# Optimization experiments

Measured on AMD Instinct MI355X. Metric: run time of the kernel, lower is better.

The kernel has to match this reference:

```python
import jax, jax.numpy as jnp
import numpy as np

K = 3  # inferred kernel size (28->26->pool->13->11->pool->5 matches 32*5*5 FC input)


def _patches(x, k=K):
    # x: (N,C,H,W) -> (N,C,k*k,OH,OW) valid patches, stride 1
    N, C, H, W = x.shape
    OH, OW = H - k + 1, W - k + 1
    return jnp.stack(
        [x[:, :, i:i + OH, j:j + OW] for i in range(k) for j in range(k)], axis=2
    )


def _maxpool2(x):
    N, C, H, W = x.shape
    H2, W2 = H // 2, W // 2
    x = x[:, :, :H2 * 2, :W2 * 2].reshape(N, C, H2, 2, W2, 2)
    return x.max(axis=(3, 5))


def _lc2d(x, w, b):
    # unshared-weight locally connected conv: w (O,C,k*k,OH,OW), b (O,OH,OW)
    p = _patches(x)  # (N,C,k*k,OH,OW)
    return jnp.einsum('nckij,ockij->noij', p, w) + b


def setup_inputs():
    key = jax.random.key(0)
    ks = jax.random.split(key, 9)
    s = 0.05
    return {
        'x': jax.random.normal(ks[0], (4096, 1, 28, 28), jnp.float32),
        'w1': jax.random.normal(ks[1], (16, 1, 9, 26, 26), jnp.float32) * s,
        'b1': jax.random.normal(ks[2], (16, 26, 26), jnp.float32) * s,
        'w2': jax.random.normal(ks[3], (32, 16, 9, 11, 11), jnp.float32) * s,
        'b2': jax.random.normal(ks[4], (32, 11, 11), jnp.float32) * s,
        'fc1_w': jax.random.normal(ks[5], (32 * 5 * 5, 128), jnp.float32) * s,
        'fc1_b': jax.random.normal(ks[6], (128,), jnp.float32) * s,
        'fc2_w': jax.random.normal(ks[7], (128, 10), jnp.float32) * s,
        'fc2_b': jax.random.normal(ks[8], (10,), jnp.float32) * s,
    }


def reference(x, w1, b1, w2, b2, fc1_w, fc1_b, fc2_w, fc2_b):
    h = _maxpool2(jax.nn.relu(_lc2d(x, w1, b1)))      # (N,16,13,13)
    h = _maxpool2(jax.nn.relu(_lc2d(h, w2, b2)))      # (N,32,5,5)
    h = h.reshape(h.shape[0], -1)                      # (N,800)
    h = jax.nn.relu(h @ fc1_w + fc1_b)                 # (N,128)
    return h @ fc2_w + fc2_b                           # (N,10)
```

## Files before the change

### kernel.cpp

```cpp
#include <hip/hip_runtime.h>

#define NB 4096

typedef __attribute__((ext_vector_type(8))) short s8v;
typedef __attribute__((ext_vector_type(4))) float f4v;

#define XB_OFF  0u
#define H1B_OFF 6422528u
#define H2B_OFF 28573696u
#define W2B_OFF 35127296u
#define B2R_OFF 36765696u
#define W1B_OFF 36778496u
#define B1R_OFF 37470720u
#define WFB_OFF 37513984u

__device__ __forceinline__ unsigned short f2bf(float f) {
  unsigned int u = __builtin_bit_cast(unsigned int, f);
  u += 0x7fffu + ((u >> 16) & 1u);
  return (unsigned short)(u >> 16);
}

__global__ __launch_bounds__(256) void k_prep(const float* __restrict__ x,
                                              const float* __restrict__ w1,
                                              const float* __restrict__ b1,
                                              const float* __restrict__ w2,
                                              const float* __restrict__ b2,
                                              const float* __restrict__ f1w,
                                              short* __restrict__ xB,
                                              short* __restrict__ w1b,
                                              float* __restrict__ b1r,
                                              short* __restrict__ w2b,
                                              float* __restrict__ b2r,
                                              short* __restrict__ wfb) {
  const int bx = blockIdx.x;
  if (bx < 3200) {
    __shared__ float t[32][33];
    const int c0 = (bx % 25) * 32;
    const int n0 = (bx / 25) * 32;
    const int tx = threadIdx.x & 31, ty = threadIdx.x >> 5;
    #pragma unroll
    for (int i = 0; i < 32; i += 8) {
      const int c = c0 + tx;
      if (c < 784) t[ty + i][tx] = x[(n0 + ty + i) * 784 + c];
    }
    __syncthreads();
    #pragma unroll
    for (int i = 0; i < 32; i += 8) {
      const int c = c0 + ty + i;
      if (c < 784) xB[c * NB + n0 + tx] = (short)f2bf(t[tx][ty + i]);
    }
  } else if (bx < 4552) {
    const int idx = (bx - 3200) * 256 + threadIdx.x;
    const int t = idx & 7;
    const int l = (idx >> 3) & 63;
    const int cv = (idx >> 9) & 3;
    const int pos = idx >> 11;
    const int k = (l >> 4) * 8 + t;
    const int o = l & 15;
    const int i = pos / 13, j = pos % 13;
    const int dy = cv >> 1, dx = cv & 1;
    float v = 0.f;
    if (k < 16) {
      const int py = k >> 2, px = k & 3;
      const int ky = py - dy, kx = px - dx;
      if (ky >= 0 && ky < 3 && kx >= 0 && kx < 3)
        v = w1[(o * 9 + ky * 3 + kx) * 676 + (2 * i + dy) * 26 + 2 * j + dx];
    }
    w1b[idx] = (short)f2bf(v);
  } else if (bx < 4595) {
    const int idx = (bx - 4552) * 256 + threadIdx.x;
    if (idx < 10816) {
      const int cv = idx & 3;
      const int o = (idx >> 2) & 15;
      const int pos = idx >> 6;
      const int i = pos / 13, j = pos % 13;
      b1r[idx] = b1[(o * 26 + 2 * i + (cv >> 1)) * 26 + 2 * j + (cv & 1)];
    }
  } else if (bx < 7795) {
    const int idx = (bx - 4595) * 256 + threadIdx.x;
    const int t = idx & 7;
    const int l = (idx >> 3) & 63;
    const int ot = (idx >> 9) & 1;
    const int s = (idx >> 10) & 7;
    const int cv = (idx >> 13) & 3;
    const int pos = idx >> 15;
    const int k = s * 32 + (l >> 4) * 8 + t;
    const int o = ot * 16 + (l & 15);
    const int w = k >> 4, c = k & 15;
    const int py = w >> 2, px = w & 3;
    const int dy = cv >> 1, dx = cv & 1;
    const int ky = py - dy, kx = px - dx;
    const int I = pos / 5, J = pos % 5;
    float v = 0.f;
    if (ky >= 0 && ky < 3 && kx >= 0 && kx < 3)
      v = w2[((o * 16 + c) * 9 + ky * 3 + kx) * 121 +
             (2 * I + dy) * 11 + (2 * J + dx)];
    w2b[idx] = (short)f2bf(v);
  } else if (bx == 7795) {
    for (int q = threadIdx.x; q < 3200; q += 256) {
      const int pos = q >> 7;
      const int r = q & 127;
      const int o = r >> 2, cv = r & 3;
      const int I = pos / 5, J = pos % 5;
      b2r[q] = b2[o * 121 + (2 * I + (cv >> 1)) * 11 + 2 * J + (cv & 1)];
    }
  } else {
    const int idx = (bx - 7796) * 256 + threadIdx.x;
    const int t = idx & 7;
    const int l = (idx >> 3) & 63;
    const int jt = (idx >> 9) & 7;
    const int s = idx >> 12;
    const int o = (l >> 4) * 8 + t;
    const int j = jt * 16 + (l & 15);
    wfb[idx] = (short)f2bf(f1w[(o * 25 + s) * 128 + j]);
  }
}

__global__ __launch_bounds__(256, 3) void k_lc1(const short* __restrict__ xB,
                                                const short* __restrict__ w1b,
                                                const float* __restrict__ b1r,
                                                short* __restrict__ h1b) {
  __shared__ short sx[16 * 264 + 16 + 8];
  __shared__ unsigned short ush[256 * 24];
  const int pos = blockIdx.y;
  const int i = pos / 13, j = pos % 13;
  const int tid = threadIdx.x;
  const int l = tid & 63;
  const int wv = tid >> 6;
  const int lm = l & 15, kg = l >> 4;
  const int n0b = blockIdx.x * 256;

  #pragma unroll
  for (int rr = 0; rr < 2; rr++) {
    const int idx = rr * 256 + tid;
    const int row = idx >> 5, seg = idx & 31;
    const int grow = (2 * i + (row >> 2)) * 28 + (2 * j + (row & 3));
    *reinterpret_cast<s8v*>(&sx[row * 264 + ((row >> 3) & 1) * 16 + seg * 8]) =
        *reinterpret_cast<const s8v*>(&xB[grow * NB + n0b + seg * 8]);
  }

  s8v bf[4];
  #pragma unroll
  for (int cv = 0; cv < 4; cv++)
    bf[cv] = *reinterpret_cast<const s8v*>(w1b + ((pos * 4 + cv) * 64 + l) * 8);
  const float4 bias = *reinterpret_cast<const float4*>(b1r + (pos * 16 + lm) * 4);
  __syncthreads();

  f4v acc[4][4];
  #pragma unroll
  for (int a = 0; a < 4; a++)
    #pragma unroll
    for (int cv = 0; cv < 4; cv++) acc[a][cv] = (f4v){0.f, 0.f, 0.f, 0.f};

  #pragma unroll
  for (int a = 0; a < 4; a++) {
    const int nl = wv * 64 + a * 16 + lm;
    s8v av = (s8v){0, 0, 0, 0, 0, 0, 0, 0};
    if (kg < 2) {
      #pragma unroll
      for (int t = 0; t < 8; t++) {
        const int k = kg * 8 + t;
        av[t] = sx[k * 264 + ((k >> 3) & 1) * 16 + nl];
      }
    }
    #pragma unroll
    for (int cv = 0; cv < 4; cv++)
      acc[a][cv] =
          __builtin_amdgcn_mfma_f32_16x16x32_bf16(av, bf[cv], acc[a][cv], 0, 0, 0);
  }

  #pragma unroll
  for (int a = 0; a < 4; a++) {
    #pragma unroll
    for (int reg = 0; reg < 4; reg++) {
      const int nl = wv * 64 + a * 16 + kg * 4 + reg;
      const float v =
          fmaxf(fmaxf(acc[a][0][reg] + bias.x, acc[a][1][reg] + bias.y),
                fmaxf(acc[a][2][reg] + bias.z, acc[a][3][reg] + bias.w));
      ush[nl * 24 + lm] = f2bf(fmaxf(v, 0.f));
    }
  }
  __syncthreads();

  short* dst = h1b + (pos * 4096 + n0b + tid) * 16;
  const unsigned short* src = ush + tid * 24;
  *reinterpret_cast<s8v*>(dst) = *reinterpret_cast<const s8v*>(src);
  *reinterpret_cast<s8v*>(dst + 8) = *reinterpret_cast<const s8v*>(src + 8);
}

__global__ __launch_bounds__(256, 4) void k_lc2(const short* __restrict__ h1b,
                                                const short* __restrict__ w2b,
                                                const float* __restrict__ b2r,
                                                short* __restrict__ h2b) {
  const int pos = blockIdx.y;
  const int I = pos / 5, J = pos % 5;
  const int tid = threadIdx.x;
  const int l = tid & 63;
  const int wave = tid >> 6;
  const int wm = wave >> 1, ot = wave & 1;
  const int n0 = blockIdx.x * 64;
  const int kg = l >> 4;
  const int lm = l & 15;
  const int c0 = (kg & 1) * 8;
  const int whalf = kg >> 1;

  f4v acc[2][4];
  #pragma unroll
  for (int a = 0; a < 2; a++)
    #pragma unroll
    for (int cv = 0; cv < 4; cv++)
      acc[a][cv] = (f4v){0.f, 0.f, 0.f, 0.f};

  #pragma unroll
  for (int s = 0; s < 8; s++) {
    const int wdw = s * 2 + whalf;
    const int py = wdw >> 2, px = wdw & 3;
    const int p = (2 * I + py) * 13 + (2 * J + px);
    const int abase = (p * 4096 + n0 + wm * 32 + lm) * 16 + c0;
    const s8v a0 = *reinterpret_cast<const s8v*>(h1b + abase);
    const s8v a1 = *reinterpret_cast<const s8v*>(h1b + abase + 16 * 16);
    #pragma unroll
    for (int cv = 0; cv < 4; cv++) {
      const s8v bf = *reinterpret_cast<const s8v*>(
          w2b + ((((pos * 4 + cv) * 8 + s) * 2 + ot) * 64 + l) * 8);
      acc[0][cv] =
          __builtin_amdgcn_mfma_f32_16x16x32_bf16(a0, bf, acc[0][cv], 0, 0, 0);
      acc[1][cv] =
          __builtin_amdgcn_mfma_f32_16x16x32_bf16(a1, bf, acc[1][cv], 0, 0, 0);
    }
  }

  const int o = ot * 16 + lm;
  const float4 bias = *reinterpret_cast<const float4*>(b2r + (pos * 32 + o) * 4);
  #pragma unroll
  for (int a = 0; a < 2; a++) {
    const int nb = n0 + wm * 32 + a * 16 + kg * 4;
    #pragma unroll
    for (int reg = 0; reg < 4; reg++) {
      const float v =
          fmaxf(fmaxf(acc[a][0][reg] + bias.x, acc[a][1][reg] + bias.y),
                fmaxf(acc[a][2][reg] + bias.z, acc[a][3][reg] + bias.w));
      h2b[(pos * 4096 + nb + reg) * 32 + o] = (short)f2bf(fmaxf(v, 0.f));
    }
  }
}

__global__ __launch_bounds__(256) void k_fc(const short* __restrict__ h2b,
                                            const short* __restrict__ wfb,
                                            const float* __restrict__ f1b,
                                            const float* __restrict__ f2w,
                                            const float* __restrict__ f2b,
                                            float* __restrict__ out) {
  __shared__ float sh3[128 * 17];
  __shared__ float swf2[128 * 12];
  __shared__ float sb1[128];
  const int tid = threadIdx.x;
  const int l = tid & 63;
  const int w = tid >> 6;
  const int lm = l & 15, kg = l >> 4;
  const int n0 = blockIdx.x * 16;
  const int jt0 = w * 2;

  for (int idx = tid; idx < 1536; idx += 256) {
    const int kk = idx / 12, f = idx % 12;
    swf2[idx] = (f < 10) ? f2w[kk * 10 + f] : 0.f;
  }
  if (tid < 128) sb1[tid] = f1b[tid];

  f4v acc0 = (f4v){0.f, 0.f, 0.f, 0.f};
  f4v acc1 = (f4v){0.f, 0.f, 0.f, 0.f};

  #pragma unroll
  for (int s = 0; s < 25; s++) {
    const s8v av = *reinterpret_cast<const s8v*>(
        h2b + (s * 4096 + n0 + lm) * 32 + kg * 8);
    const s8v b0 = *reinterpret_cast<const s8v*>(
        wfb + ((s * 8 + jt0) * 64 + l) * 8);
    const s8v b1v = *reinterpret_cast<const s8v*>(
        wfb + ((s * 8 + jt0 + 1) * 64 + l) * 8);
    acc0 = __builtin_amdgcn_mfma_f32_16x16x32_bf16(av, b0, acc0, 0, 0, 0);
    acc1 = __builtin_amdgcn_mfma_f32_16x16x32_bf16(av, b1v, acc1, 0, 0, 0);
  }
  __syncthreads();

  #pragma unroll
  for (int q = 0; q < 2; q++) {
    const f4v a = q ? acc1 : acc0;
    const int j = (jt0 + q) * 16 + lm;
    #pragma unroll
    for (int reg = 0; reg < 4; reg++)
      sh3[j * 17 + kg * 4 + reg] = fmaxf(a[reg] + sb1[j], 0.f);
  }
  __syncthreads();

  if (tid < 160) {
    const int oo = tid >> 4, nn = tid & 15;
    float s = f2b[oo];
    for (int j = 0; j < 128; j++)
      s += sh3[j * 17 + nn] * swf2[j * 12 + oo];
    out[(n0 + nn) * 10 + oo] = s;
  }
}

extern "C" void kernel_launch(void* const* d_in, const int* in_sizes, int n_in,
                              void* d_out, int out_size, void* d_ws,
                              size_t ws_size, hipStream_t stream) {
  const float* x   = (const float*)d_in[0];
  const float* w1  = (const float*)d_in[1];
  const float* b1  = (const float*)d_in[2];
  const float* w2  = (const float*)d_in[3];
  const float* b2  = (const float*)d_in[4];
  const float* f1w = (const float*)d_in[5];
  const float* f1b = (const float*)d_in[6];
  const float* f2w = (const float*)d_in[7];
  const float* f2b = (const float*)d_in[8];
  float* out = (float*)d_out;
  char* ws = (char*)d_ws;
  short* xB  = (short*)(ws + XB_OFF);
  short* h1b = (short*)(ws + H1B_OFF);
  short* h2b = (short*)(ws + H2B_OFF);
  short* w2b = (short*)(ws + W2B_OFF);
  float* b2r = (float*)(ws + B2R_OFF);
  short* w1b = (short*)(ws + W1B_OFF);
  float* b1r = (float*)(ws + B1R_OFF);
  short* wfb = (short*)(ws + WFB_OFF);

  k_prep<<<8196, 256, 0, stream>>>(x, w1, b1, w2, b2, f1w,
                                   xB, w1b, b1r, w2b, b2r, wfb);
  k_lc1<<<dim3(16, 169), 256, 0, stream>>>(xB, w1b, b1r, h1b);
  k_lc2<<<dim3(64, 25), 256, 0, stream>>>(h1b, w2b, b2r, h2b);
  k_fc<<<256, 256, 0, stream>>>(h2b, wfb, f1b, f2w, f2b, out);
}
```

Measured before the change: 120.3 us.

## Widen prep transpose with vectorized stores and double batch tile per lc2 wave

The input transpose in k_prep now handles 64 batch rows per block and writes eight packed bf16 values per thread as one 16-byte store instead of scalar short stores, halving the transpose block count. k_lc2 gives each wave 64 batch rows (four 16-row MFMA tiles) instead of 32, so each loaded weight fragment feeds twice as many MFMAs and the grid is halved. The cost is more accumulator registers per thread and fewer blocks, which may lower occupancy on lc2.

After: 118.2 us. No clear change (-1.7%).

```diff
diff --git a/kernel.cpp b/kernel.cpp
--- a/kernel.cpp
+++ b/kernel.cpp
@@ -33,24 +33,27 @@
                                               float* __restrict__ b2r,
                                               short* __restrict__ wfb) {
   const int bx = blockIdx.x;
-  if (bx < 3200) {
-    __shared__ float t[32][33];
+  if (bx < 1600) {
+    __shared__ float t2[64][33];
     const int c0 = (bx % 25) * 32;
-    const int n0 = (bx / 25) * 32;
+    const int n0 = (bx / 25) * 64;
     const int tx = threadIdx.x & 31, ty = threadIdx.x >> 5;
-    #pragma unroll
-    for (int i = 0; i < 32; i += 8) {
-      const int c = c0 + tx;
-      if (c < 784) t[ty + i][tx] = x[(n0 + ty + i) * 784 + c];
-    }
+    const int c = c0 + tx;
+    #pragma unroll
+    for (int i = 0; i < 64; i += 8)
+      if (c < 784) t2[ty + i][tx] = x[(n0 + ty + i) * 784 + c];
     __syncthreads();
-    #pragma unroll
-    for (int i = 0; i < 32; i += 8) {
-      const int c = c0 + ty + i;
-      if (c < 784) xB[c * NB + n0 + tx] = (short)f2bf(t[tx][ty + i]);
-    }
-  } else if (bx < 4552) {
-    const int idx = (bx - 3200) * 256 + threadIdx.x;
+    const int cl = threadIdx.x >> 3;
+    const int ns = (threadIdx.x & 7) * 8;
+    if (c0 + cl < 784) {
+      unsigned short v[8];
+      #pragma unroll
+      for (int q = 0; q < 8; q++) v[q] = f2bf(t2[ns + q][cl]);
+      *reinterpret_cast<s8v*>(&xB[(c0 + cl) * NB + n0 + ns]) =
+          *reinterpret_cast<const s8v*>(v);
+    }
+  } else if (bx < 2952) {
+    const int idx = (bx - 1600) * 256 + threadIdx.x;
     const int t = idx & 7;
     const int l = (idx >> 3) & 63;
     const int cv = (idx >> 9) & 3;
@@ -67,8 +70,8 @@
         v = w1[(o * 9 + ky * 3 + kx) * 676 + (2 * i + dy) * 26 + 2 * j + dx];
     }
     w1b[idx] = (short)f2bf(v);
-  } else if (bx < 4595) {
-    const int idx = (bx - 4552) * 256 + threadIdx.x;
+  } else if (bx < 2995) {
+    const int idx = (bx - 2952) * 256 + threadIdx.x;
     if (idx < 10816) {
       const int cv = idx & 3;
       const int o = (idx >> 2) & 15;
@@ -76,8 +79,8 @@
       const int i = pos / 13, j = pos % 13;
       b1r[idx] = b1[(o * 26 + 2 * i + (cv >> 1)) * 26 + 2 * j + (cv & 1)];
     }
-  } else if (bx < 7795) {
-    const int idx = (bx - 4595) * 256 + threadIdx.x;
+  } else if (bx < 6195) {
+    const int idx = (bx - 2995) * 256 + threadIdx.x;
     const int t = idx & 7;
     const int l = (idx >> 3) & 63;
     const int ot = (idx >> 9) & 1;
@@ -96,7 +99,7 @@
       v = w2[((o * 16 + c) * 9 + ky * 3 + kx) * 121 +
              (2 * I + dy) * 11 + (2 * J + dx)];
     w2b[idx] = (short)f2bf(v);
-  } else if (bx == 7795) {
+  } else if (bx == 6195) {
     for (int q = threadIdx.x; q < 3200; q += 256) {
       const int pos = q >> 7;
       const int r = q & 127;
@@ -105,7 +108,7 @@
       b2r[q] = b2[o * 121 + (2 * I + (cv >> 1)) * 11 + 2 * J + (cv & 1)];
     }
   } else {
-    const int idx = (bx - 7796) * 256 + threadIdx.x;
+    const int idx = (bx - 6196) * 256 + threadIdx.x;
     const int t = idx & 7;
     const int l = (idx >> 3) & 63;
     const int jt = (idx >> 9) & 7;
@@ -198,15 +201,15 @@
   const int l = tid & 63;
   const int wave = tid >> 6;
   const int wm = wave >> 1, ot = wave & 1;
-  const int n0 = blockIdx.x * 64;
+  const int nw = blockIdx.x * 128 + wm * 64;
   const int kg = l >> 4;
   const int lm = l & 15;
   const int c0 = (kg & 1) * 8;
   const int whalf = kg >> 1;
 
-  f4v acc[2][4];
-  #pragma unroll
-  for (int a = 0; a < 2; a++)
+  f4v acc[4][4];
+  #pragma unroll
+  for (int a = 0; a < 4; a++)
     #pragma unroll
     for (int cv = 0; cv < 4; cv++)
       acc[a][cv] = (f4v){0.f, 0.f, 0.f, 0.f};
@@ -216,25 +219,27 @@
     const int wdw = s * 2 + whalf;
     const int py = wdw >> 2, px = wdw & 3;
     const int p = (2 * I + py) * 13 + (2 * J + px);
-    const int abase = (p * 4096 + n0 + wm * 32 + lm) * 16 + c0;
-    const s8v a0 = *reinterpret_cast<const s8v*>(h1b + abase);
-    const s8v a1 = *reinterpret_cast<const s8v*>(h1b + abase + 16 * 16);
+    const int abase = (p * 4096 + nw + lm) * 16 + c0;
+    s8v av[4];
+    #pragma unroll
+    for (int a = 0; a < 4; a++)
+      av[a] = *reinterpret_cast<const s8v*>(h1b + abase + a * 256);
     #pragma unroll
     for (int cv = 0; cv < 4; cv++) {
       const s8v bf = *reinterpret_cast<const s8v*>(
           w2b + ((((pos * 4 + cv) * 8 + s) * 2 + ot) * 64 + l) * 8);
-      acc[0][cv] =
-          __builtin_amdgcn_mfma_f32_16x16x32_bf16(a0, bf, acc[0][cv], 0, 0, 0);
-      acc[1][cv] =
-          __builtin_amdgcn_mfma_f32_16x16x32_bf16(a1, bf, acc[1][cv], 0, 0, 0);
+      #pragma unroll
+      for (int a = 0; a < 4; a++)
+        acc[a][cv] =
+            __builtin_amdgcn_mfma_f32_16x16x32_bf16(av[a], bf, acc[a][cv], 0, 0, 0);
     }
   }
 
   const int o = ot * 16 + lm;
   const float4 bias = *reinterpret_cast<const float4*>(b2r + (pos * 32 + o) * 4);
   #pragma unroll
-  for (int a = 0; a < 2; a++) {
-    const int nb = n0 + wm * 32 + a * 16 + kg * 4;
+  for (int a = 0; a < 4; a++) {
+    const int nb = nw + a * 16 + kg * 4;
     #pragma unroll
     for (int reg = 0; reg < 4; reg++) {
       const float v =
@@ -325,9 +330,9 @@
   float* b1r = (float*)(ws + B1R_OFF);
   short* wfb = (short*)(ws + WFB_OFF);
 
-  k_prep<<<8196, 256, 0, stream>>>(x, w1, b1, w2, b2, f1w,
+  k_prep<<<6596, 256, 0, stream>>>(x, w1, b1, w2, b2, f1w,
                                    xB, w1b, b1r, w2b, b2r, wfb);
   k_lc1<<<dim3(16, 169), 256, 0, stream>>>(xB, w1b, b1r, h1b);
-  k_lc2<<<dim3(64, 25), 256, 0, stream>>>(h1b, w2b, b2r, h2b);
+  k_lc2<<<dim3(32, 25), 256, 0, stream>>>(h1b, w2b, b2r, h2b);
   k_fc<<<256, 256, 0, stream>>>(h2b, wfb, f1b, f2w, f2b, out);
 }
```
